# Kernel tuning notes

Measured on AMD Instinct MI355X. Metric: run time of the kernel, lower is better.

The kernel has to match this reference:

```python
import jax, jax.numpy as jnp
import numpy as np

B, C_IN, H, W = 2048, 192, 19, 19
G1, P1 = 32, 32

def setup_inputs() -> dict:
    key = jax.random.key(0)
    ks = jax.random.split(key, 10)
    inputs = jax.random.normal(ks[0], (B, C_IN, H, W), dtype=jnp.float32)
    # binary validity mask (most points valid), plus its per-sample sum
    mask = (jax.random.uniform(ks[1], (B, 1, H, W)) > 0.1).astype(jnp.float32)
    mask_sum_hw = jnp.sum(mask, axis=(2, 3), keepdims=True)  # [B,1,1,1]
    s = 0.05
    return {
        "inputs": inputs,
        "mask": mask,
        "mask_sum_hw": mask_sum_hw,
        "w1p": jax.random.normal(ks[2], (P1, C_IN), dtype=jnp.float32) * s,
        "b1p": jnp.zeros((P1,), jnp.float32),
        "w1g": jax.random.normal(ks[3], (G1, C_IN), dtype=jnp.float32) * s,
        "b1g": jnp.zeros((G1,), jnp.float32),
        "beta_g": jnp.zeros((1, G1, 1, 1), jnp.float32),
        "w_lin": jax.random.normal(ks[4], (P1, 3 * G1), dtype=jnp.float32) * s,
        "b_lin": jnp.zeros((P1,), jnp.float32),
        "beta2": jnp.zeros((1, P1, 1, 1), jnp.float32),
        "w2p": jax.random.normal(ks[5], (1, P1), dtype=jnp.float32) * s,
        "b2p": jnp.zeros((1,), jnp.float32),
    }

def _conv1x1(x, w, b):
    # x: [B,C,H,W], w: [O,C] -> [B,O,H,W]
    return jnp.einsum('bchw,oc->bohw', x, w) + b[None, :, None, None]

def _gpool(x, mask, mask_sum_hw):
    # x: [B,G,H,W]; returns [B,3G,1,1]
    off = (jnp.sqrt(mask_sum_hw) - 28.0) / 10.0
    mean = jnp.sum(x, axis=(2, 3), keepdims=True) / mask_sum_hw
    mx = jnp.max(x + (mask - 1.0), axis=(2, 3), keepdims=True)
    return jnp.concatenate([mean, mean * off, mx], axis=1)

def reference(inputs, mask, mask_sum_hw, w1p, b1p, w1g, b1g, beta_g,
              w_lin, b_lin, beta2, w2p, b2p):
    b, _, h, w = inputs.shape
    outp = _conv1x1(inputs, w1p, b1p)                      # [B,P1,H,W]
    outg = _conv1x1(inputs, w1g, b1g)                      # [B,G1,H,W]
    outg = (outg + beta_g) * mask                          # NormMask (no gamma)
    outg = jax.nn.gelu(outg, approximate=False)            # torch GELU = exact erf
    outg = _gpool(outg, mask, mask_sum_hw)                 # [B,3G1,1,1]
    outg = outg.reshape(b, -1) @ w_lin.T + b_lin           # [B,P1]
    outp = outp + outg[:, :, None, None]
    outp = (outp + beta2) * mask                           # NormMask
    outp = jax.nn.gelu(outp, approximate=False)
    outp = _conv1x1(outp, w2p, b2p)                        # [B,1,H,W]
    outp = outp - (1.0 - mask) * 5000.0
    outp = jax.nn.log_softmax(outp.reshape(b, -1), axis=1)
    return outp.reshape(b, h, w)
```

## Files before the change

kernel.cpp:

```cpp
#include <hip/hip_runtime.h>
#include <hip/hip_bf16.h>
#include <math.h>

#define NB   2048
#define CIN  192
#define HW   361
#define NTH  512
#define WPAD 200

typedef float f32x4 __attribute__((ext_vector_type(4)));
typedef short s16x8 __attribute__((ext_vector_type(8)));

__device__ __forceinline__ short f2bf_bits(float f) {
    __hip_bfloat16 h = __float2bfloat16(f);
    short s;
    __builtin_memcpy(&s, &h, sizeof(s));
    return s;
}

__device__ __forceinline__ float gelu_fast(float x) {
    float inner = x * fmaf(0.044715f, x * x, 1.0f);
    float t = 1.5957691216057308f * inner;
    if (t > 40.f) return x;
    float e = __expf(t);
    return x * (e / (e + 1.0f));
}

__global__ __launch_bounds__(NTH, 4)
void policy_head_mfma(const float* __restrict__ inputs,
                      const float* __restrict__ mask,
                      const float* __restrict__ mask_sum,
                      const float* __restrict__ w1p, const float* __restrict__ b1p,
                      const float* __restrict__ w1g, const float* __restrict__ b1g,
                      const float* __restrict__ beta_g,
                      const float* __restrict__ w_lin, const float* __restrict__ b_lin,
                      const float* __restrict__ beta2,
                      const float* __restrict__ w2p, const float* __restrict__ b2p,
                      float* __restrict__ out) {
    __shared__ unsigned short wlds[64 * WPAD];
    __shared__ float small[160];
    __shared__ float redA[32 * 8];
    __shared__ float redB[32 * 8];
    __shared__ float pooled[96];
    __shared__ float linout[32];

    const int tid = threadIdx.x;
    const int b   = blockIdx.x;

    for (int i = tid; i < 64 * CIN; i += NTH) {
        int o = i / CIN, c = i - o * CIN;
        float wv = (o < 32) ? w1p[o * CIN + c] : w1g[(o - 32) * CIN + c];
        wlds[o * WPAD + c] = (unsigned short)f2bf_bits(wv);
    }
    if (tid < 32)       small[tid] = b1p[tid];
    else if (tid < 64)  small[tid] = b1g[tid - 32];
    else if (tid < 96)  small[tid] = beta_g[tid - 64];
    else if (tid < 128) small[tid] = beta2[tid - 96];
    else if (tid < 160) small[tid] = w2p[tid - 128];
    __syncthreads();

    const int w    = tid >> 6;
    const int lane = tid & 63;
    const int g4   = lane >> 4;
    const int c16  = lane & 15;
    const int krow = 8 * g4;

    int   px[3], pxc[3];
    float mv[3];
    bool  valid[3];
    #pragma unroll
    for (int nt = 0; nt < 3; ++nt) {
        px[nt]    = w * 48 + nt * 16 + c16;
        valid[nt] = (px[nt] < HW);
        pxc[nt]   = valid[nt] ? px[nt] : (HW - 1);
        mv[nt]    = valid[nt] ? mask[(size_t)b * HW + px[nt]] : 0.f;
    }

    const float* xb = inputs + (size_t)b * (CIN * HW);

    auto loadx = [&](float (&xv)[3][8], int kk) {
        const float* xk = xb + (size_t)(kk * 32 + krow) * HW;
        #pragma unroll
        for (int nt = 0; nt < 3; ++nt) {
            const float* xp = xk + pxc[nt];
            #pragma unroll
            for (int i = 0; i < 8; ++i) xv[nt][i] = xp[i * HW];
        }
    };

    f32x4 acc[4][3];
    #pragma unroll
    for (int mt = 0; mt < 4; ++mt)
        #pragma unroll
        for (int nt = 0; nt < 3; ++nt)
            acc[mt][nt] = (f32x4){0.f, 0.f, 0.f, 0.f};

    float xv[3][8];
    loadx(xv, 0);

    for (int kk = 0; kk < 6; ++kk) {
        s16x8 bfr[3];
        #pragma unroll
        for (int nt = 0; nt < 3; ++nt)
            #pragma unroll
            for (int i = 0; i < 8; ++i)
                bfr[nt][i] = f2bf_bits(xv[nt][i]);

        int kkn = (kk < 5) ? kk + 1 : 0;
        loadx(xv, kkn);

        s16x8 a[4];
        #pragma unroll
        for (int mt = 0; mt < 4; ++mt)
            a[mt] = *(const s16x8*)&wlds[(mt * 16 + c16) * WPAD + kk * 32 + krow];

        #pragma unroll
        for (int nt = 0; nt < 3; ++nt)
            #pragma unroll
            for (int mt = 0; mt < 4; ++mt)
                acc[mt][nt] = __builtin_amdgcn_mfma_f32_16x16x32_bf16(a[mt], bfr[nt], acc[mt][nt], 0, 0, 0);
    }

    const float ms  = mask_sum[b];
    const float off = (sqrtf(ms) - 28.0f) * 0.1f;

    #pragma unroll
    for (int mt = 2; mt < 4; ++mt) {
        #pragma unroll
        for (int r = 0; r < 4; ++r) {
            int og = (mt - 2) * 16 + g4 * 4 + r;
            float bb = small[32 + og] + small[64 + og];
            float s = 0.f, mx = -1e30f;
            #pragma unroll
            for (int nt = 0; nt < 3; ++nt) {
                float v = gelu_fast((acc[mt][nt][r] + bb) * mv[nt]);
                if (!valid[nt]) v = 0.f;
                s += v;
                float cand = valid[nt] ? (v + mv[nt] - 1.f) : -1e30f;
                mx = fmaxf(mx, cand);
            }
            #pragma unroll
            for (int o = 1; o < 16; o <<= 1) {
                s += __shfl_xor(s, o, 64);
                mx = fmaxf(mx, __shfl_xor(mx, o, 64));
            }
            if (c16 == 0) { redA[og * 8 + w] = s; redB[og * 8 + w] = mx; }
        }
    }
    __syncthreads();

    if (tid < 32) {
        float s = 0.f, mx = -1e30f;
        #pragma unroll
        for (int j = 0; j < 8; ++j) {
            s += redA[tid * 8 + j];
            mx = fmaxf(mx, redB[tid * 8 + j]);
        }
        float mean = s / ms;
        pooled[tid]      = mean;
        pooled[32 + tid] = mean * off;
        pooled[64 + tid] = mx;
    }
    __syncthreads();

    if (tid < 32) {
        float a = b_lin[tid];
        #pragma unroll
        for (int j = 0; j < 96; ++j) a = fmaf(pooled[j], w_lin[tid * 96 + j], a);
        linout[tid] = a;
    }
    __syncthreads();

    float pv[3] = {0.f, 0.f, 0.f};
    #pragma unroll
    for (int mt = 0; mt < 2; ++mt) {
        #pragma unroll
        for (int r = 0; r < 4; ++r) {
            int op = mt * 16 + g4 * 4 + r;
            float bb = small[op] + linout[op] + small[96 + op];
            float wo = small[128 + op];
            #pragma unroll
            for (int nt = 0; nt < 3; ++nt)
                pv[nt] += gelu_fast((acc[mt][nt][r] + bb) * mv[nt]) * wo;
        }
    }
    const float b2 = b2p[0];
    float logit[3];
    #pragma unroll
    for (int nt = 0; nt < 3; ++nt) {
        float t = pv[nt];
        t += __shfl_xor(t, 16, 64);
        t += __shfl_xor(t, 32, 64);
        logit[nt] = t + b2 - (1.f - mv[nt]) * 5000.f;
    }

    float lmax = -1e30f;
    #pragma unroll
    for (int nt = 0; nt < 3; ++nt)
        if (valid[nt]) lmax = fmaxf(lmax, logit[nt]);
    #pragma unroll
    for (int o = 1; o < 64; o <<= 1) lmax = fmaxf(lmax, __shfl_xor(lmax, o, 64));
    if (lane == 0) redA[w] = lmax;
    __syncthreads();
    float gmax = -1e30f;
    #pragma unroll
    for (int j = 0; j < 8; ++j) gmax = fmaxf(gmax, redA[j]);

    float es = 0.f;
    #pragma unroll
    for (int nt = 0; nt < 3; ++nt)
        if (valid[nt] && g4 == 0) es += __expf(logit[nt] - gmax);
    #pragma unroll
    for (int o = 1; o < 64; o <<= 1) es += __shfl_xor(es, o, 64);
    if (lane == 0) redB[w] = es;
    __syncthreads();
    float tot = 0.f;
    #pragma unroll
    for (int j = 0; j < 8; ++j) tot += redB[j];
    const float lt = __logf(tot) + gmax;

    if (g4 == 0) {
        #pragma unroll
        for (int nt = 0; nt < 3; ++nt)
            if (valid[nt]) out[(size_t)b * HW + px[nt]] = logit[nt] - lt;
    }
}

extern "C" void kernel_launch(void* const* d_in, const int* in_sizes, int n_in,
                              void* d_out, int out_size, void* d_ws, size_t ws_size,
                              hipStream_t stream) {
    const float* inputs   = (const float*)d_in[0];
    const float* mask     = (const float*)d_in[1];
    const float* mask_sum = (const float*)d_in[2];
    const float* w1p      = (const float*)d_in[3];
    const float* b1p      = (const float*)d_in[4];
    const float* w1g      = (const float*)d_in[5];
    const float* b1g      = (const float*)d_in[6];
    const float* beta_g   = (const float*)d_in[7];
    const float* w_lin    = (const float*)d_in[8];
    const float* b_lin    = (const float*)d_in[9];
    const float* beta2    = (const float*)d_in[10];
    const float* w2p      = (const float*)d_in[11];
    const float* b2p      = (const float*)d_in[12];
    float* out = (float*)d_out;

    policy_head_mfma<<<dim3(NB), dim3(NTH), 0, stream>>>(
        inputs, mask, mask_sum, w1p, b1p, w1g, b1g, beta_g,
        w_lin, b_lin, beta2, w2p, b2p, out);
}
```

Measured before the change: 156.7 us.

## Stage input tiles through swizzled LDS with vectorized float4 global loads

Input activations are now loaded with 16-byte vector loads along the pixel dimension, packed into bf16 pairs, and written to a transposed, XOR-swizzled LDS tile. MFMA B-fragments are then read from LDS as single 16-byte loads instead of eight strided scalar global loads per fragment. Weight staging also switches to float4 loads with packed bf16 writes. The aim is better global coalescing and fewer load instructions, at the cost of two block-wide barriers per K step and extra LDS traffic.

```diff
diff --git a/kernel.cpp b/kernel.cpp
--- a/kernel.cpp
+++ b/kernel.cpp
@@ -6,16 +6,19 @@
 #define CIN  192
 #define HW   361
 #define NTH  512
-#define WPAD 200
-
-typedef float f32x4 __attribute__((ext_vector_type(4)));
-typedef short s16x8 __attribute__((ext_vector_type(8)));
-
-__device__ __forceinline__ short f2bf_bits(float f) {
+
+typedef float  f32x4  __attribute__((ext_vector_type(4)));
+typedef short  s16x8  __attribute__((ext_vector_type(8)));
+typedef float  f32x4u __attribute__((ext_vector_type(4), aligned(4)));
+
+__device__ __forceinline__ unsigned short f2bf_bits(float f) {
     __hip_bfloat16 h = __float2bfloat16(f);
-    short s;
+    unsigned short s;
     __builtin_memcpy(&s, &h, sizeof(s));
     return s;
+}
+__device__ __forceinline__ unsigned int packbf(float lo, float hi) {
+    return (unsigned int)f2bf_bits(lo) | ((unsigned int)f2bf_bits(hi) << 16);
 }
 
 __device__ __forceinline__ float gelu_fast(float x) {
@@ -37,56 +40,92 @@
                       const float* __restrict__ beta2,
                       const float* __restrict__ w2p, const float* __restrict__ b2p,
                       float* __restrict__ out) {
-    __shared__ unsigned short wlds[64 * WPAD];
+    __shared__ unsigned int wlds32[64 * 100];
+    __shared__ unsigned int xt32[384 * 16];
     __shared__ float small[160];
-    __shared__ float redA[32 * 8];
-    __shared__ float redB[32 * 8];
+    __shared__ float redA[256];
+    __shared__ float redB[256];
     __shared__ float pooled[96];
     __shared__ float linout[32];
 
-    const int tid = threadIdx.x;
-    const int b   = blockIdx.x;
-
-    for (int i = tid; i < 64 * CIN; i += NTH) {
-        int o = i / CIN, c = i - o * CIN;
-        float wv = (o < 32) ? w1p[o * CIN + c] : w1g[(o - 32) * CIN + c];
-        wlds[o * WPAD + c] = (unsigned short)f2bf_bits(wv);
+    const int tid  = threadIdx.x;
+    const int b    = blockIdx.x;
+    const int w    = tid >> 6;
+    const int lane = tid & 63;
+    const int g4   = lane >> 4;
+    const int c16  = lane & 15;
+
+    const float* xb = inputs + (size_t)b * (CIN * HW);
+
+    const int p   = ((w & 3) << 2) + (lane >> 4);
+    const int gl  = lane & 15;
+    const int W2  = w >> 2;
+    int gs[3];
+    #pragma unroll
+    for (int k = 0; k < 3; ++k) gs[k] = W2 * 16 + 32 * k + gl;
+
+    float va[3][4], vb[3][4];
+
+    auto loadx = [&](int kk) {
+        const float* tb = xb + (size_t)(kk * 32 + 2 * p) * HW;
+        #pragma unroll
+        for (int k = 0; k < 3; ++k) {
+            int g = gs[k];
+            if (g <= 89) {
+                f32x4u r0 = *(const f32x4u*)(tb + 4 * g);
+                f32x4u r1 = *(const f32x4u*)(tb + HW + 4 * g);
+                #pragma unroll
+                for (int j = 0; j < 4; ++j) { va[k][j] = r0[j]; vb[k][j] = r1[j]; }
+            } else if (g == 90) {
+                va[k][0] = tb[360];
+                vb[k][0] = tb[HW + 360];
+            }
+        }
+    };
+
+    auto write_xt = [&]() {
+        #pragma unroll
+        for (int k = 0; k < 3; ++k) {
+            int g  = gs[k];
+            int qb = (((p >> 2) ^ (g & 3)) << 2) | (p & 3);
+            if (g <= 89) {
+                #pragma unroll
+                for (int j = 0; j < 4; ++j)
+                    xt32[(4 * g + j) * 16 + qb] = packbf(va[k][j], vb[k][j]);
+            } else if (g == 90) {
+                xt32[360 * 16 + qb] = packbf(va[k][0], vb[k][0]);
+            }
+        }
+    };
+
+    loadx(0);
+
+    #pragma unroll
+    for (int k = 0; k < 6; ++k) {
+        int i = tid + k * NTH;
+        int o = i / 48, cq = i - o * 48;
+        const float* src = (o < 32) ? (w1p + o * CIN + 4 * cq)
+                                    : (w1g + (o - 32) * CIN + 4 * cq);
+        float4 v = *(const float4*)src;
+        wlds32[o * 100 + 2 * cq]     = packbf(v.x, v.y);
+        wlds32[o * 100 + 2 * cq + 1] = packbf(v.z, v.w);
     }
     if (tid < 32)       small[tid] = b1p[tid];
     else if (tid < 64)  small[tid] = b1g[tid - 32];
     else if (tid < 96)  small[tid] = beta_g[tid - 64];
     else if (tid < 128) small[tid] = beta2[tid - 96];
     else if (tid < 160) small[tid] = w2p[tid - 128];
-    __syncthreads();
-
-    const int w    = tid >> 6;
-    const int lane = tid & 63;
-    const int g4   = lane >> 4;
-    const int c16  = lane & 15;
-    const int krow = 8 * g4;
-
-    int   px[3], pxc[3];
+
+    int   px[3], bidx[3];
     float mv[3];
     bool  valid[3];
     #pragma unroll
     for (int nt = 0; nt < 3; ++nt) {
         px[nt]    = w * 48 + nt * 16 + c16;
         valid[nt] = (px[nt] < HW);
-        pxc[nt]   = valid[nt] ? px[nt] : (HW - 1);
         mv[nt]    = valid[nt] ? mask[(size_t)b * HW + px[nt]] : 0.f;
-    }
-
-    const float* xb = inputs + (size_t)b * (CIN * HW);
-
-    auto loadx = [&](float (&xv)[3][8], int kk) {
-        const float* xk = xb + (size_t)(kk * 32 + krow) * HW;
-        #pragma unroll
-        for (int nt = 0; nt < 3; ++nt) {
-            const float* xp = xk + pxc[nt];
-            #pragma unroll
-            for (int i = 0; i < 8; ++i) xv[nt][i] = xp[i * HW];
-        }
-    };
+        bidx[nt]  = px[nt] * 16 + ((g4 ^ (c16 >> 2)) << 2);
+    }
 
     f32x4 acc[4][3];
     #pragma unroll
@@ -95,30 +134,26 @@
         for (int nt = 0; nt < 3; ++nt)
             acc[mt][nt] = (f32x4){0.f, 0.f, 0.f, 0.f};
 
-    float xv[3][8];
-    loadx(xv, 0);
+    __syncthreads();
 
     for (int kk = 0; kk < 6; ++kk) {
+        write_xt();
+        __syncthreads();
+        if (kk < 5) loadx(kk + 1);
+
         s16x8 bfr[3];
         #pragma unroll
         for (int nt = 0; nt < 3; ++nt)
-            #pragma unroll
-            for (int i = 0; i < 8; ++i)
-                bfr[nt][i] = f2bf_bits(xv[nt][i]);
-
-        int kkn = (kk < 5) ? kk + 1 : 0;
-        loadx(xv, kkn);
-
-        s16x8 a[4];
-        #pragma unroll
-        for (int mt = 0; mt < 4; ++mt)
-            a[mt] = *(const s16x8*)&wlds[(mt * 16 + c16) * WPAD + kk * 32 + krow];
-
-        #pragma unroll
-        for (int nt = 0; nt < 3; ++nt)
-            #pragma unroll
-            for (int mt = 0; mt < 4; ++mt)
-                acc[mt][nt] = __builtin_amdgcn_mfma_f32_16x16x32_bf16(a[mt], bfr[nt], acc[mt][nt], 0, 0, 0);
+            bfr[nt] = *(const s16x8*)&xt32[bidx[nt]];
+
+        #pragma unroll
+        for (int mt = 0; mt < 4; ++mt) {
+            s16x8 a = *(const s16x8*)&wlds32[(mt * 16 + c16) * 100 + kk * 16 + 4 * g4];
+            #pragma unroll
+            for (int nt = 0; nt < 3; ++nt)
+                acc[mt][nt] = __builtin_amdgcn_mfma_f32_16x16x32_bf16(a, bfr[nt], acc[mt][nt], 0, 0, 0);
+        }
+        if (kk < 5) __syncthreads();
     }
 
     const float ms  = mask_sum[b];
```

Measured after the change: 195.8 us. +25.0%, slower.

## Persistent blocks stream inputs via async global-to-LDS double buffering

Applied to the files above, without the earlier changes.

Replaces the one-block-per-sample launch with 256 blocks that each process 8 samples. Each 32-channel input slab is staged into double-buffered LDS with global_load_lds, so the next chunk's load overlaps the current MFMA work. Weights, the transposed w_lin, the masks and the small parameters are loaded once per block, which amortises their setup across samples. In exchange the grid shrinks to 256 blocks with larger LDS use (occupancy 2), and the loop now has more barriers per stage.

```diff
diff --git a/kernel.cpp b/kernel.cpp
--- a/kernel.cpp
+++ b/kernel.cpp
@@ -2,20 +2,27 @@
 #include <hip/hip_bf16.h>
 #include <math.h>
 
-#define NB   2048
-#define CIN  192
-#define HW   361
-#define NTH  512
-#define WPAD 200
+#define NBLK   256
+#define EPB    8
+#define CIN    192
+#define HW     361
+#define NTH    512
+#define NSTAGE 48
+#define TILE_BYTES 46208
+#define SLOTS  2888
+#define PSLOTS 3072
 
 typedef float f32x4 __attribute__((ext_vector_type(4)));
 typedef short s16x8 __attribute__((ext_vector_type(8)));
 
-__device__ __forceinline__ short f2bf_bits(float f) {
+__device__ __forceinline__ unsigned short f2bf_bits(float f) {
     __hip_bfloat16 h = __float2bfloat16(f);
-    short s;
+    unsigned short s;
     __builtin_memcpy(&s, &h, sizeof(s));
     return s;
+}
+__device__ __forceinline__ unsigned int packbf(float lo, float hi) {
+    return (unsigned int)f2bf_bits(lo) | ((unsigned int)f2bf_bits(hi) << 16);
 }
 
 __device__ __forceinline__ float gelu_fast(float x) {
@@ -26,8 +33,12 @@
     return x * (e / (e + 1.0f));
 }
 
-__global__ __launch_bounds__(NTH, 4)
-void policy_head_mfma(const float* __restrict__ inputs,
+#define GLD_LDS16(g, l) __builtin_amdgcn_global_load_lds( \
+    (const __attribute__((address_space(1))) unsigned int*)(g), \
+    (__attribute__((address_space(3))) unsigned int*)(l), 16, 0, 0)
+
+__global__ __launch_bounds__(NTH, 2)
+void policy_head_pipe(const float* __restrict__ inputs,
                       const float* __restrict__ mask,
                       const float* __restrict__ mask_sum,
                       const float* __restrict__ w1p, const float* __restrict__ b1p,
@@ -37,192 +48,243 @@
                       const float* __restrict__ beta2,
                       const float* __restrict__ w2p, const float* __restrict__ b2p,
                       float* __restrict__ out) {
-    __shared__ unsigned short wlds[64 * WPAD];
-    __shared__ float small[160];
-    __shared__ float redA[32 * 8];
-    __shared__ float redB[32 * 8];
-    __shared__ float pooled[96];
-    __shared__ float linout[32];
-
-    const int tid = threadIdx.x;
-    const int b   = blockIdx.x;
-
-    for (int i = tid; i < 64 * CIN; i += NTH) {
-        int o = i / CIN, c = i - o * CIN;
-        float wv = (o < 32) ? w1p[o * CIN + c] : w1g[(o - 32) * CIN + c];
-        wlds[o * WPAD + c] = (unsigned short)f2bf_bits(wv);
-    }
-    if (tid < 32)       small[tid] = b1p[tid];
-    else if (tid < 64)  small[tid] = b1g[tid - 32];
-    else if (tid < 96)  small[tid] = beta_g[tid - 64];
-    else if (tid < 128) small[tid] = beta2[tid - 96];
-    else if (tid < 160) small[tid] = w2p[tid - 128];
-    __syncthreads();
-
-    const int w    = tid >> 6;
+    __shared__ __align__(16) float xbuf[2][PSLOTS * 4];
+    __shared__ unsigned int wlds[64 * 100];
+    __shared__ float wlin_t[96 * 32];
+    __shared__ float mlds[EPB * HW];
+    __shared__ float small[224];
+    __shared__ float redA[256], redB[256], pooled[96], linout[32];
+
+    const int tid  = threadIdx.x;
+    const int bid  = blockIdx.x;
+    const int wv   = tid >> 6;
     const int lane = tid & 63;
     const int g4   = lane >> 4;
     const int c16  = lane & 15;
-    const int krow = 8 * g4;
-
-    int   px[3], pxc[3];
-    float mv[3];
-    bool  valid[3];
+
+    int px[3], pxc[3];
+    bool valid[3];
     #pragma unroll
     for (int nt = 0; nt < 3; ++nt) {
-        px[nt]    = w * 48 + nt * 16 + c16;
+        px[nt]    = wv * 48 + nt * 16 + c16;
         valid[nt] = (px[nt] < HW);
         pxc[nt]   = valid[nt] ? px[nt] : (HW - 1);
-        mv[nt]    = valid[nt] ? mask[(size_t)b * HW + px[nt]] : 0.f;
-    }
-
-    const float* xb = inputs + (size_t)b * (CIN * HW);
-
-    auto loadx = [&](float (&xv)[3][8], int kk) {
-        const float* xk = xb + (size_t)(kk * 32 + krow) * HW;
+    }
+
+    #pragma unroll
+    for (int k = 0; k < 6; ++k) {
+        int i = tid + k * NTH;
+        int o = i / 48, cq = i - o * 48;
+        const float* src = (o < 32) ? (w1p + o * CIN + 4 * cq)
+                                    : (w1g + (o - 32) * CIN + 4 * cq);
+        float4 v = *(const float4*)src;
+        wlds[o * 100 + 2 * cq]     = packbf(v.x, v.y);
+        wlds[o * 100 + 2 * cq + 1] = packbf(v.z, v.w);
+    }
+    #pragma unroll
+    for (int k = 0; k < 6; ++k) {
+        int i = tid + k * NTH;
+        int j = i >> 5, o = i & 31;
+        wlin_t[i] = w_lin[o * 96 + j];
+    }
+    #pragma unroll
+    for (int k = 0; k < 6; ++k) {
+        int i = tid + k * NTH;
+        if (i < EPB * HW) mlds[i] = mask[(size_t)bid * EPB * HW + i];
+    }
+    if (tid < 32)        small[tid] = b1p[tid];
+    else if (tid < 64)   small[tid] = b1g[tid - 32];
+    else if (tid < 96)   small[tid] = beta_g[tid - 64];
+    else if (tid < 128)  small[tid] = beta2[tid - 96];
+    else if (tid < 160)  small[tid] = w2p[tid - 128];
+    else if (tid < 192)  small[tid] = b_lin[tid - 160];
+    else if (tid < 200)  small[tid] = mask_sum[bid * EPB + (tid - 192)];
+    else if (tid == 200) small[tid] = b2p[0];
+
+    __syncthreads();
+
+    const char* in_base = (const char*)inputs;
+    auto stage_gll = [&](int t, int pb) {
+        const char* src = in_base + ((size_t)(bid * EPB + t / 6) * CIN * HW
+                                     + (size_t)(t % 6) * 32 * HW) * 4;
         #pragma unroll
-        for (int nt = 0; nt < 3; ++nt) {
-            const float* xp = xk + pxc[nt];
-            #pragma unroll
-            for (int i = 0; i < 8; ++i) xv[nt][i] = xp[i * HW];
+        for (int j = 0; j < 6; ++j) {
+            int slotbase = (j * 8 + wv) * 64;
+            int cs = slotbase + lane;
+            if (cs > SLOTS - 1) cs = SLOTS - 1;
+            GLD_LDS16(src + (size_t)cs * 16, &xbuf[pb][slotbase * 4]);
         }
     };
 
     f32x4 acc[4][3];
-    #pragma unroll
-    for (int mt = 0; mt < 4; ++mt)
-        #pragma unroll
-        for (int nt = 0; nt < 3; ++nt)
-            acc[mt][nt] = (f32x4){0.f, 0.f, 0.f, 0.f};
-
-    float xv[3][8];
-    loadx(xv, 0);
-
-    for (int kk = 0; kk < 6; ++kk) {
-        s16x8 bfr[3];
-        #pragma unroll
-        for (int nt = 0; nt < 3; ++nt)
-            #pragma unroll
-            for (int i = 0; i < 8; ++i)
-                bfr[nt][i] = f2bf_bits(xv[nt][i]);
-
-        int kkn = (kk < 5) ? kk + 1 : 0;
-        loadx(xv, kkn);
-
-        s16x8 a[4];
-        #pragma unroll
-        for (int mt = 0; mt < 4; ++mt)
-            a[mt] = *(const s16x8*)&wlds[(mt * 16 + c16) * WPAD + kk * 32 + krow];
-
-        #pragma unroll
-        for (int nt = 0; nt < 3; ++nt)
+
+    stage_gll(0, 0);
+    stage_gll(1, 1);
+    asm volatile("s_waitcnt vmcnt(6)" ::: "memory");
+    __builtin_amdgcn_s_barrier();
+
+    auto lbar = [] {
+        asm volatile("s_waitcnt lgkmcnt(0)" ::: "memory");
+        __builtin_amdgcn_s_barrier();
+    };
+
+    for (int t = 0; t < NSTAGE; ++t) {
+        const int pb = t & 1;
+        const int kk = t % 6;
+
+        if (kk == 0) {
             #pragma unroll
             for (int mt = 0; mt < 4; ++mt)
-                acc[mt][nt] = __builtin_amdgcn_mfma_f32_16x16x32_bf16(a[mt], bfr[nt], acc[mt][nt], 0, 0, 0);
-    }
-
-    const float ms  = mask_sum[b];
-    const float off = (sqrtf(ms) - 28.0f) * 0.1f;
-
-    #pragma unroll
-    for (int mt = 2; mt < 4; ++mt) {
-        #pragma unroll
-        for (int r = 0; r < 4; ++r) {
-            int og = (mt - 2) * 16 + g4 * 4 + r;
-            float bb = small[32 + og] + small[64 + og];
-            float s = 0.f, mx = -1e30f;
+                #pragma unroll
+                for (int nt = 0; nt < 3; ++nt)
+                    acc[mt][nt] = (f32x4){0.f, 0.f, 0.f, 0.f};
+        }
+
+        {
+            const float* xf = xbuf[pb];
+            s16x8 bfr[3];
             #pragma unroll
             for (int nt = 0; nt < 3; ++nt) {
-                float v = gelu_fast((acc[mt][nt][r] + bb) * mv[nt]);
-                if (!valid[nt]) v = 0.f;
-                s += v;
-                float cand = valid[nt] ? (v + mv[nt] - 1.f) : -1e30f;
-                mx = fmaxf(mx, cand);
-            }
-            #pragma unroll
-            for (int o = 1; o < 16; o <<= 1) {
-                s += __shfl_xor(s, o, 64);
-                mx = fmaxf(mx, __shfl_xor(mx, o, 64));
-            }
-            if (c16 == 0) { redA[og * 8 + w] = s; redB[og * 8 + w] = mx; }
-        }
-    }
-    __syncthreads();
-
-    if (tid < 32) {
-        float s = 0.f, mx = -1e30f;
-        #pragma unroll
-        for (int j = 0; j < 8; ++j) {
-            s += redA[tid * 8 + j];
-            mx = fmaxf(mx, redB[tid * 8 + j]);
-        }
-        float mean = s / ms;
-        pooled[tid]      = mean;
-        pooled[32 + tid] = mean * off;
-        pooled[64 + tid] = mx;
-    }
-    __syncthreads();
-
-    if (tid < 32) {
-        float a = b_lin[tid];
-        #pragma unroll
-        for (int j = 0; j < 96; ++j) a = fmaf(pooled[j], w_lin[tid * 96 + j], a);
-        linout[tid] = a;
-    }
-    __syncthreads();
-
-    float pv[3] = {0.f, 0.f, 0.f};
-    #pragma unroll
-    for (int mt = 0; mt < 2; ++mt) {
-        #pragma unroll
-        for (int r = 0; r < 4; ++r) {
-            int op = mt * 16 + g4 * 4 + r;
-            float bb = small[op] + linout[op] + small[96 + op];
-            float wo = small[128 + op];
+                float v[8];
+                #pragma unroll
+                for (int i = 0; i < 8; ++i)
+                    v[i] = xf[(8 * g4 + i) * HW + pxc[nt]];
+                #pragma unroll
+                for (int i = 0; i < 8; ++i)
+                    bfr[nt][i] = (short)f2bf_bits(v[i]);
+            }
+            #pragma unroll
+            for (int mt = 0; mt < 4; ++mt) {
+                s16x8 a = *(const s16x8*)&wlds[(mt * 16 + c16) * 100 + kk * 16 + 4 * g4];
+                #pragma unroll
+                for (int nt = 0; nt < 3; ++nt)
+                    acc[mt][nt] = __builtin_amdgcn_mfma_f32_16x16x32_bf16(a, bfr[nt], acc[mt][nt], 0, 0, 0);
+            }
+        }
+
+        asm volatile("" ::: "memory");
+        __builtin_amdgcn_s_barrier();
+
+        if (t + 2 < NSTAGE) {
+            stage_gll(t + 2, pb);
+            asm volatile("s_waitcnt vmcnt(6)" ::: "memory");
+        } else {
+            asm volatile("s_waitcnt vmcnt(0)" ::: "memory");
+        }
+        __builtin_amdgcn_s_barrier();
+
+        if (kk == 5) {
+            const int e = t / 6;
+            const float ms  = small[192 + e];
+            const float off = (sqrtf(ms) - 28.0f) * 0.1f;
+            float mv[3];
             #pragma unroll
             for (int nt = 0; nt < 3; ++nt)
-                pv[nt] += gelu_fast((acc[mt][nt][r] + bb) * mv[nt]) * wo;
-        }
-    }
-    const float b2 = b2p[0];
-    float logit[3];
-    #pragma unroll
-    for (int nt = 0; nt < 3; ++nt) {
-        float t = pv[nt];
-        t += __shfl_xor(t, 16, 64);
-        t += __shfl_xor(t, 32, 64);
-        logit[nt] = t + b2 - (1.f - mv[nt]) * 5000.f;
-    }
-
-    float lmax = -1e30f;
-    #pragma unroll
-    for (int nt = 0; nt < 3; ++nt)
-        if (valid[nt]) lmax = fmaxf(lmax, logit[nt]);
-    #pragma unroll
-    for (int o = 1; o < 64; o <<= 1) lmax = fmaxf(lmax, __shfl_xor(lmax, o, 64));
-    if (lane == 0) redA[w] = lmax;
-    __syncthreads();
-    float gmax = -1e30f;
-    #pragma unroll
-    for (int j = 0; j < 8; ++j) gmax = fmaxf(gmax, redA[j]);
-
-    float es = 0.f;
-    #pragma unroll
-    for (int nt = 0; nt < 3; ++nt)
-        if (valid[nt] && g4 == 0) es += __expf(logit[nt] - gmax);
-    #pragma unroll
-    for (int o = 1; o < 64; o <<= 1) es += __shfl_xor(es, o, 64);
-    if (lane == 0) redB[w] = es;
-    __syncthreads();
-    float tot = 0.f;
-    #pragma unroll
-    for (int j = 0; j < 8; ++j) tot += redB[j];
-    const float lt = __logf(tot) + gmax;
-
-    if (g4 == 0) {
-        #pragma unroll
-        for (int nt = 0; nt < 3; ++nt)
-            if (valid[nt]) out[(size_t)b * HW + px[nt]] = logit[nt] - lt;
+                mv[nt] = valid[nt] ? mlds[e * HW + pxc[nt]] : 0.f;
+
+            #pragma unroll
+            for (int mt = 2; mt < 4; ++mt) {
+                #pragma unroll
+                for (int r = 0; r < 4; ++r) {
+                    int og = (mt - 2) * 16 + g4 * 4 + r;
+                    float bb = small[32 + og] + small[64 + og];
+                    float s = 0.f, mx = -1e30f;
+                    #pragma unroll
+                    for (int nt = 0; nt < 3; ++nt) {
+                        float v = gelu_fast((acc[mt][nt][r] + bb) * mv[nt]);
+                        if (!valid[nt]) v = 0.f;
+                        s += v;
+                        float cand = valid[nt] ? (v + mv[nt] - 1.f) : -1e30f;
+                        mx = fmaxf(mx, cand);
+                    }
+                    #pragma unroll
+                    for (int o = 1; o < 16; o <<= 1) {
+                        s += __shfl_xor(s, o, 64);
+                        mx = fmaxf(mx, __shfl_xor(mx, o, 64));
+                    }
+                    if (c16 == 0) { redA[og * 8 + wv] = s; redB[og * 8 + wv] = mx; }
+                }
+            }
+            lbar();
+
+            if (tid < 32) {
+                float s = 0.f, mx = -1e30f;
+                #pragma unroll
+                for (int j = 0; j < 8; ++j) {
+                    s += redA[tid * 8 + j];
+                    mx = fmaxf(mx, redB[tid * 8 + j]);
+                }
+                float mean = s / ms;
+                pooled[tid]      = mean;
+                pooled[32 + tid] = mean * off;
+                pooled[64 + tid] = mx;
+            }
+            lbar();
+
+            if (tid < 32) {
+                float a = small[160 + tid];
+                #pragma unroll
+                for (int j = 0; j < 96; ++j) a = fmaf(pooled[j], wlin_t[j * 32 + tid], a);
+                linout[tid] = a;
+            }
+            lbar();
+
+            float pv[3] = {0.f, 0.f, 0.f};
+            #pragma unroll
+            for (int mt = 0; mt < 2; ++mt) {
+                #pragma unroll
+                for (int r = 0; r < 4; ++r) {
+                    int op = mt * 16 + g4 * 4 + r;
+                    float bb = small[op] + linout[op] + small[96 + op];
+                    float wo = small[128 + op];
+                    #pragma unroll
+                    for (int nt = 0; nt < 3; ++nt)
+                        pv[nt] += gelu_fast((acc[mt][nt][r] + bb) * mv[nt]) * wo;
+                }
+            }
+            const float b2 = small[200];
+            float logit[3];
+            #pragma unroll
+            for (int nt = 0; nt < 3; ++nt) {
+                float s = pv[nt];
+                s += __shfl_xor(s, 16, 64);
+                s += __shfl_xor(s, 32, 64);
+                logit[nt] = s + b2 - (1.f - mv[nt]) * 5000.f;
+            }
+
+            float lmax = -1e30f;
+            #pragma unroll
+            for (int nt = 0; nt < 3; ++nt)
+                if (valid[nt]) lmax = fmaxf(lmax, logit[nt]);
+            #pragma unroll
+            for (int o = 1; o < 64; o <<= 1) lmax = fmaxf(lmax, __shfl_xor(lmax, o, 64));
+            if (lane == 0) redA[wv] = lmax;
+            lbar();
+            float gmax = -1e30f;
+            #pragma unroll
+            for (int j = 0; j < 8; ++j) gmax = fmaxf(gmax, redA[j]);
+
+            float es = 0.f;
+            #pragma unroll
+            for (int nt = 0; nt < 3; ++nt)
+                if (valid[nt] && g4 == 0) es += __expf(logit[nt] - gmax);
+            #pragma unroll
+            for (int o = 1; o < 64; o <<= 1) es += __shfl_xor(es, o, 64);
+            if (lane == 0) redB[wv] = es;
+            lbar();
+            float tot = 0.f;
+            #pragma unroll
+            for (int j = 0; j < 8; ++j) tot += redB[j];
+            const float lt = __logf(tot) + gmax;
+
+            if (g4 == 0) {
+                #pragma unroll
+                for (int nt = 0; nt < 3; ++nt)
+                    if (valid[nt])
+                        out[((size_t)bid * EPB + e) * HW + px[nt]] = logit[nt] - lt;
+            }
+            lbar();
+        }
     }
 }
 
@@ -244,7 +306,7 @@
     const float* b2p      = (const float*)d_in[12];
     float* out = (float*)d_out;
 
-    policy_head_mfma<<<dim3(NB), dim3(NTH), 0, stream>>>(
+    policy_head_pipe<<<dim3(NBLK), dim3(NTH), 0, stream>>>(
         inputs, mask, mask_sum, w1p, b1p, w1g, b1g, beta_g,
         w_lin, b_lin, beta2, w2p, b2p, out);
 }
```

Result: slower. 173.7 us (+10.8%).
